# Kernel optimization log

Measured on AMD Instinct MI355X. Metric: run time of the kernel, lower is better.

Reference implementation:

```python
import jax, jax.numpy as jnp
import numpy as np

N = 100000   # nodes
E = 3200000  # edges
IN = 5
H = 128
L = 6
EPS = 1e-5

def _bn(x, g, b):
    # BatchNorm1d in training mode: batch stats over node dim, biased variance
    m = jnp.mean(x, axis=0)
    v = jnp.mean((x - m) ** 2, axis=0)
    return (x - m) * jax.lax.rsqrt(v + EPS) * g + b

def setup_inputs() -> dict:
    key = jax.random.key(0)
    ks = jax.random.split(key, 20)
    x = jax.random.normal(ks[0], (N, IN), dtype=jnp.float32)
    edge_index = jax.random.randint(ks[1], (2, E), 0, N, dtype=jnp.int64)
    batch = jnp.zeros((N,), dtype=jnp.int64)
    s = 0.05
    return {
        "x": x, "edge_index": edge_index, "batch": batch,
        "in_W": jax.random.normal(ks[2], (IN, H), jnp.float32) * s,
        "in_b": jnp.zeros((H,), jnp.float32),
        "in_g": jnp.ones((H,), jnp.float32),
        "in_beta": jnp.zeros((H,), jnp.float32),
        "conv_W": jax.random.normal(ks[3], (L, H, H), jnp.float32) * s,
        "conv_b": jnp.zeros((L, H), jnp.float32),
        "bn_g": jnp.ones((L, H), jnp.float32),
        "bn_beta": jnp.zeros((L, H), jnp.float32),
        "pW1": jax.random.normal(ks[4], (H, 32), jnp.float32) * s,
        "pb1": jnp.zeros((32,), jnp.float32),
        "pW2": jax.random.normal(ks[5], (32, 1), jnp.float32) * s,
        "pb2": jnp.zeros((1,), jnp.float32),
        "vW1": jax.random.normal(ks[6], (H, 64), jnp.float32) * s,
        "vb1": jnp.zeros((64,), jnp.float32),
        "vW2": jax.random.normal(ks[7], (64, 1), jnp.float32) * s,
        "vb2": jnp.zeros((1,), jnp.float32),
    }

def reference(x, edge_index, batch, in_W, in_b, in_g, in_beta,
              conv_W, conv_b, bn_g, bn_beta,
              pW1, pb1, pW2, pb2, vW1, vb1, vW2, vb2):
    n = x.shape[0]
    # GCN normalization with self-loops (computed once; depends only on edge_index)
    loops = jnp.arange(n, dtype=edge_index.dtype)
    src = jnp.concatenate([edge_index[0], loops])
    dst = jnp.concatenate([edge_index[1], loops])
    deg = jax.ops.segment_sum(jnp.ones_like(dst, dtype=x.dtype), dst, num_segments=n)
    dinv = jnp.where(deg > 0, jax.lax.rsqrt(deg), 0.0)
    norm = dinv[src] * dinv[dst]  # [E+N]

    def gcn(h, W, b):
        h = h @ W
        msg = h[src] * norm[:, None]
        return jax.ops.segment_sum(msg, dst, num_segments=n) + b

    h = jax.nn.relu(_bn(x @ in_W + in_b, in_g, in_beta))
    for i in range(L):
        h = jax.nn.relu(_bn(gcn(h, conv_W[i], conv_b[i]), bn_g[i], bn_beta[i])) + h

    policy_logits = (jax.nn.relu(h @ pW1 + pb1) @ pW2 + pb2)[:, 0]  # [N]

    # global_mean_pool over batch ids (single graph here, num_segments=1)
    num_graphs = 1
    sums = jax.ops.segment_sum(h, batch, num_segments=num_graphs)
    cnts = jax.ops.segment_sum(jnp.ones((n,), h.dtype), batch, num_segments=num_graphs)
    g = sums / jnp.maximum(cnts, 1.0)[:, None]  # [1, H]
    value = jnp.tanh(jax.nn.relu(g @ vW1 + vb1) @ vW2 + vb2)[:, 0]  # [1]
    return policy_logits, value
```

## Files before the change

kernel.cpp:

```cpp
#include <hip/hip_runtime.h>
#include <hip/hip_bf16.h>

typedef __hip_bfloat16 bf16;
typedef long long i64;
typedef unsigned short u16;
typedef __attribute__((ext_vector_type(8))) short bf16x8;
typedef __attribute__((ext_vector_type(4))) float f32x4;

#define EPSV 1e-5f
#define WINLEN 2560
#define CHUNK 64

static __device__ __forceinline__ float ldf(const void* p, size_t i, int fb) {
  return fb ? __bfloat162float(((const bf16*)p)[i]) : ((const float*)p)[i];
}
static __device__ __forceinline__ u16 f2b(float f) {
  unsigned int u = __float_as_uint(f);
  u += 0x7FFF + ((u >> 16) & 1);
  return (u16)(u >> 16);
}
static __device__ __forceinline__ float rb2f(u16 u) {
  return __uint_as_float(((unsigned int)u) << 16);
}


__global__ void setup_kernel(const int* __restrict__ ei_w, const unsigned int* __restrict__ g,
                             int* __restrict__ eflag, int* __restrict__ fflag,
                             int* __restrict__ degcnt, int* __restrict__ fill,
                             int* __restrict__ wctr, int n) {
  int i = blockIdx.x * 256 + threadIdx.x;
  if (i < n) { degcnt[i] = 0; fill[i] = 0; }
  if (blockIdx.x == 0) {
    __shared__ int nz;
    if (threadIdx.x == 0) nz = 0;
    if (threadIdx.x < 32) wctr[threadIdx.x] = 0;
    __syncthreads();
    for (int k = threadIdx.x; k < 1024; k += 256)
      if (ei_w[2 * k + 1] != 0) atomicAdd(&nz, 1);
    __syncthreads();
    if (threadIdx.x == 0) {
      *eflag = (nz == 0) ? 1 : 0;
      *fflag = (g[0] == 0x3F803F80u) ? 1 : 0;
    }
  }
}

__global__ void deg_kernel(const void* __restrict__ ei, const int* __restrict__ flag,
                           int* __restrict__ degcnt, int e, int n) {
  int k = blockIdx.x & 7;
  int lo = (int)(((long long)n * k) >> 3);
  int hi = (int)(((long long)n * (k + 1)) >> 3);
  int stride = (gridDim.x >> 3) * 256;
  int fb64 = *flag;
  for (int i = (blockIdx.x >> 3) * 256 + threadIdx.x; i < e; i += stride) {
    int d;
    if (fb64) d = (int)((const i64*)ei)[(size_t)e + i];
    else      d = ((const int*)ei)[(size_t)e + i];
    if (d >= lo && d < hi) atomicAdd(&degcnt[d], 1);
  }
}


__global__ void __launch_bounds__(256) scanA_kernel(const int* __restrict__ deg,
                                                    int* __restrict__ rp,
                                                    int* __restrict__ bsum,
                                                    float* __restrict__ dinv, int n) {
  int base = blockIdx.x * 1024 + threadIdx.x * 4;
  int v0 = (base     < n) ? deg[base]     : 0;
  int v1 = (base + 1 < n) ? deg[base + 1] : 0;
  int v2 = (base + 2 < n) ? deg[base + 2] : 0;
  int v3 = (base + 3 < n) ? deg[base + 3] : 0;
  if (base     < n) dinv[base]     = rsqrtf((float)v0 + 1.0f);
  if (base + 1 < n) dinv[base + 1] = rsqrtf((float)v1 + 1.0f);
  if (base + 2 < n) dinv[base + 2] = rsqrtf((float)v2 + 1.0f);
  if (base + 3 < n) dinv[base + 3] = rsqrtf((float)v3 + 1.0f);
  int ts = v0 + v1 + v2 + v3;
  __shared__ int ls[256];
  ls[threadIdx.x] = ts;
  __syncthreads();
  for (int off = 1; off < 256; off <<= 1) {
    int u = (threadIdx.x >= off) ? ls[threadIdx.x - off] : 0;
    __syncthreads();
    ls[threadIdx.x] += u;
    __syncthreads();
  }
  int run = ls[threadIdx.x] - ts;
  if (base     < n) rp[base]     = run; run += v0;
  if (base + 1 < n) rp[base + 1] = run; run += v1;
  if (base + 2 < n) rp[base + 2] = run; run += v2;
  if (base + 3 < n) rp[base + 3] = run;
  if (threadIdx.x == 255) bsum[blockIdx.x] = ls[255];
}

__global__ void __launch_bounds__(256) scanB_kernel(int* __restrict__ bsum, int* __restrict__ rp,
                                                    int nb, int n, int e) {
  __shared__ int ls[256];
  int t = threadIdx.x;
  int v = (t < nb) ? bsum[t] : 0;
  ls[t] = v;
  __syncthreads();
  for (int off = 1; off < 256; off <<= 1) {
    int u = (t >= off) ? ls[t - off] : 0;
    __syncthreads();
    ls[t] += u;
    __syncthreads();
  }
  if (t < nb) bsum[t] = ls[t] - v;
  if (t == 0) rp[n] = e;
}

__global__ void scanC_kernel(int* __restrict__ rp, const int* __restrict__ bsum, int n) {
  int i = blockIdx.x * 256 + threadIdx.x;
  if (i < n) rp[i] += bsum[i >> 10];
}

__global__ void fill_kernel(const void* __restrict__ ei, const int* __restrict__ flag,
                            const int* __restrict__ row_ptr,
                            int* __restrict__ fill, int* __restrict__ csr_src, int e, int n) {
  int k = blockIdx.x & 7;
  int lo = (int)(((long long)n * k) >> 3);
  int hi = (int)(((long long)n * (k + 1)) >> 3);
  int stride = (gridDim.x >> 3) * 256;
  int fb64 = *flag;
  for (int i = (blockIdx.x >> 3) * 256 + threadIdx.x; i < e; i += stride) {
    int d;
    if (fb64) d = (int)((const i64*)ei)[(size_t)e + i];
    else      d = ((const int*)ei)[(size_t)e + i];
    if (d < lo || d >= hi) continue;
    int s;
    if (fb64) s = (int)((const i64*)ei)[i];
    else      s = ((const int*)ei)[i];
    int pos = row_ptr[d] + atomicAdd(&fill[d], 1);
    csr_src[pos] = s;
  }
}


__global__ void wfrag_kernel(const void* __restrict__ W, const int* __restrict__ fflag,
                             u16* __restrict__ wf, int total) {
  int fb = *fflag;
  int i = blockIdx.x * 256 + threadIdx.x;
  if (i >= total) return;
  int l = i >> 14, r = i & 16383;
  int k = r >> 7, nn = r & 127;
  int s = k >> 5, quad = (k >> 3) & 3, j = k & 7;
  int ct = nn >> 4, n16 = nn & 15;
  wf[(size_t)l * 16384 + (ct * 4 + s) * 512 + quad * 128 + n16 * 8 + j] = f2b(ldf(W, i, fb));
}


__global__ void __launch_bounds__(256) inproj_stats_kernel(
    const void* __restrict__ x, const void* __restrict__ W, const void* __restrict__ b,
    const int* __restrict__ fflag, float* __restrict__ pre,
    float* __restrict__ pi, int n, int in_dim) {
  int fb = *fflag;
  int q = threadIdx.x & 31, g8 = threadIdx.x >> 5;
  int c = q * 4;
  float b0 = ldf(b, c, fb), b1 = ldf(b, c + 1, fb), b2v = ldf(b, c + 2, fb), b3 = ldf(b, c + 3, fb);
  float s0 = 0, s1 = 0, s2 = 0, s3 = 0, q0 = 0, q1 = 0, q2 = 0, q3 = 0;
  for (int node = blockIdx.x * 8 + g8; node < n; node += gridDim.x * 8) {
    float a0 = b0, a1 = b1, a2 = b2v, a3 = b3;
    for (int k = 0; k < in_dim; ++k) {
      float xv = ldf(x, (size_t)node * in_dim + k, fb);
      size_t w0 = (size_t)k * 128 + c;
      a0 = fmaf(xv, ldf(W, w0, fb), a0);
      a1 = fmaf(xv, ldf(W, w0 + 1, fb), a1);
      a2 = fmaf(xv, ldf(W, w0 + 2, fb), a2);
      a3 = fmaf(xv, ldf(W, w0 + 3, fb), a3);
    }
    *(float4*)(pre + (size_t)node * 128 + c) = make_float4(a0, a1, a2, a3);
    s0 += a0; s1 += a1; s2 += a2; s3 += a3;
    q0 = fmaf(a0, a0, q0); q1 = fmaf(a1, a1, q1); q2 = fmaf(a2, a2, q2); q3 = fmaf(a3, a3, q3);
  }
  __shared__ float4 SS[256], QQ[256];
  SS[threadIdx.x] = make_float4(s0, s1, s2, s3);
  QQ[threadIdx.x] = make_float4(q0, q1, q2, q3);
  __syncthreads();
  if (threadIdx.x < 32) {
    float4 a = SS[threadIdx.x], qq = QQ[threadIdx.x];
    for (int g = 1; g < 8; ++g) {
      float4 u = SS[g * 32 + threadIdx.x], w = QQ[g * 32 + threadIdx.x];
      a.x += u.x; a.y += u.y; a.z += u.z; a.w += u.w;
      qq.x += w.x; qq.y += w.y; qq.z += w.z; qq.w += w.w;
    }
    int cc = threadIdx.x * 4;
    *(float4*)(pi + (size_t)blockIdx.x * 256 + cc) = a;
    *(float4*)(pi + (size_t)blockIdx.x * 256 + 128 + cc) = qq;
  }
}

__global__ void __launch_bounds__(1024) finalize_inproj_kernel(
    const float* __restrict__ pi, int nb,
    const void* __restrict__ g, const void* __restrict__ beta,
    const int* __restrict__ fflag,
    float* __restrict__ scale, float* __restrict__ shift,
    float inv_n) {
  __shared__ float RS[8][128], RQ[8][128];
  int fb = *fflag;
  int c = threadIdx.x & 127, r = threadIdx.x >> 7;
  float s = 0.f, s2 = 0.f;
#pragma unroll 4
  for (int b = r; b < nb; b += 8) {
    s  += pi[(size_t)b * 256 + c];
    s2 += pi[(size_t)b * 256 + 128 + c];
  }
  RS[r][c] = s; RQ[r][c] = s2;
  __syncthreads();
  if (threadIdx.x < 128) {
    float ts = 0.f, tq = 0.f;
#pragma unroll
    for (int i = 0; i < 8; ++i) { ts += RS[i][c]; tq += RQ[i][c]; }
    float mean = ts * inv_n;
    float var = tq * inv_n - mean * mean;
    float sc = ldf(g, c, fb) * rsqrtf(var + EPSV);
    scale[c] = sc;
    shift[c] = ldf(beta, c, fb) - mean * sc;
  }
}


__global__ void __launch_bounds__(256) gemm_bn_kernel(
    const float* __restrict__ pre, float* __restrict__ hbuf,
    const float* __restrict__ scale, const float* __restrict__ shift,
    const u16* __restrict__ wfL, const float* __restrict__ dinv,
    u16* __restrict__ u, int n, int use_res) {
  __shared__ u16 At[4][2048];
  int lane = threadIdx.x & 63;
  int wave = threadIdx.x >> 6;
  int n16 = lane & 15, quad = lane >> 4;
  u16* at = At[wave];
  int node = lane & 15;
  int cgrp = lane >> 4;
  int ntiles = (n + 15) >> 4;
  for (int tile = blockIdx.x * 4 + wave; tile < ntiles; tile += gridDim.x * 4) {
    int n0 = tile * 16;
    int gn = n0 + node;
#pragma unroll
    for (int r = 0; r < 8; ++r) {
      int c4 = r * 4 + cgrp;
      int c = c4 * 4;
      float4 h4 = make_float4(0.f, 0.f, 0.f, 0.f);
      if (gn < n) {
        float4 p = *(const float4*)(pre + (size_t)gn * 128 + c);
        float4 sc = *(const float4*)(scale + c);
        float4 sh = *(const float4*)(shift + c);
        h4.x = fmaxf(fmaf(p.x, sc.x, sh.x), 0.f);
        h4.y = fmaxf(fmaf(p.y, sc.y, sh.y), 0.f);
        h4.z = fmaxf(fmaf(p.z, sc.z, sh.z), 0.f);
        h4.w = fmaxf(fmaf(p.w, sc.w, sh.w), 0.f);
        if (use_res) {
          float4 rv = *(const float4*)(hbuf + (size_t)gn * 128 + c);
          h4.x += rv.x; h4.y += rv.y; h4.z += rv.z; h4.w += rv.w;
        }
        *(float4*)(hbuf + (size_t)gn * 128 + c) = h4;
      }
      ushort4 uu;
      uu.x = f2b(h4.x); uu.y = f2b(h4.y); uu.z = f2b(h4.z); uu.w = f2b(h4.w);
      int s = c4 >> 3, qd = (c4 >> 1) & 3, j0 = (c4 & 1) * 4;
      *(ushort4*)(at + s * 512 + qd * 128 + node * 8 + j0) = uu;
    }
    __builtin_amdgcn_s_waitcnt(0);
    f32x4 acc[8];
#pragma unroll
    for (int ct = 0; ct < 8; ++ct) acc[ct] = (f32x4){0.f, 0.f, 0.f, 0.f};
#pragma unroll
    for (int s = 0; s < 4; ++s) {
      bf16x8 af = *(const bf16x8*)(at + s * 512 + lane * 8);
#pragma unroll
      for (int ct = 0; ct < 8; ++ct) {
        bf16x8 bfr = *(const bf16x8*)(wfL + (size_t)(ct * 4 + s) * 512 + lane * 8);
        acc[ct] = __builtin_amdgcn_mfma_f32_16x16x32_bf16(af, bfr, acc[ct], 0, 0, 0);
      }
    }
    float dv[4];
#pragma unroll
    for (int r = 0; r < 4; ++r) {
      int row = n0 + quad * 4 + r;
      dv[r] = (row < n) ? dinv[row] : 0.f;
    }
#pragma unroll
    for (int ct = 0; ct < 8; ++ct) {
#pragma unroll
      for (int r = 0; r < 4; ++r) {
        int row = n0 + quad * 4 + r;
        if (row < n)
          u[((size_t)(ct >> 1) * n + row) * 32 + (ct & 1) * 16 + n16] = f2b(acc[ct][r] * dv[r]);
      }
    }
  }
}


__global__ void __launch_bounds__(256) gather_stats_kernel(
    const int* __restrict__ row_ptr, const int* __restrict__ csr_src,
    const u16* __restrict__ u, const float* __restrict__ dinv,
    const void* __restrict__ b, const int* __restrict__ fflag,
    float* __restrict__ pre, float* __restrict__ pg,
    int* __restrict__ wctr, int n, int nch, size_t bOff) {
  __shared__ int sm[WINLEN];
  __shared__ float SW[4][4][8], QW[4][4][8];
  __shared__ int curchunk;
  int fb = *fflag;
  int ct2 = blockIdx.x & 3;
  const u16* us = u + (size_t)ct2 * n * 32;
  int q = threadIdx.x & 3;
  int g = threadIdx.x >> 2;
  int c = ct2 * 32 + q * 8;
  float bias[8];
#pragma unroll
  for (int i = 0; i < 8; ++i) bias[i] = ldf(b, bOff + c + i, fb);
  float sA[8], qA[8];
#pragma unroll
  for (int i = 0; i < 8; ++i) { sA[i] = 0.f; qA[i] = 0.f; }

  for (;;) {
    __syncthreads();
    if (threadIdx.x == 0) curchunk = atomicAdd(&wctr[ct2], 1);
    __syncthreads();
    int ch = curchunk;
    if (ch >= nch) break;
    int c0 = ch * CHUNK;
    int node = c0 + g;
    int valid = node < n;
    int beg = valid ? row_ptr[node] : 0;
    int end = valid ? row_ptr[node + 1] : 0;
    int cend = c0 + CHUNK; if (cend > n) cend = n;
    int chunk_lo = row_ptr[c0];
    int chunk_hi = row_ptr[cend];
    float acc[8];
    if (valid) {
      uint4 su = *(const uint4*)(us + (size_t)node * 32 + q * 8);
      acc[0] = __uint_as_float(su.x << 16); acc[1] = __uint_as_float(su.x & 0xFFFF0000u);
      acc[2] = __uint_as_float(su.y << 16); acc[3] = __uint_as_float(su.y & 0xFFFF0000u);
      acc[4] = __uint_as_float(su.z << 16); acc[5] = __uint_as_float(su.z & 0xFFFF0000u);
      acc[6] = __uint_as_float(su.w << 16); acc[7] = __uint_as_float(su.w & 0xFFFF0000u);
    } else {
#pragma unroll
      for (int i = 0; i < 8; ++i) acc[i] = 0.f;
    }
    for (int wlo = chunk_lo; wlo < chunk_hi; wlo += WINLEN) {
      int wlen = chunk_hi - wlo; if (wlen > WINLEN) wlen = WINLEN;
      __syncthreads();
      for (int i = threadIdx.x; i < wlen; i += 256)
        sm[i] = __builtin_nontemporal_load(csr_src + wlo + i);
      __syncthreads();
      int j0 = beg > wlo ? beg : wlo;
      int j1 = end < wlo + wlen ? end : wlo + wlen;
      int j = j0;
#define ACC(UU) \
      acc[0] += __uint_as_float(UU.x << 16); acc[1] += __uint_as_float(UU.x & 0xFFFF0000u); \
      acc[2] += __uint_as_float(UU.y << 16); acc[3] += __uint_as_float(UU.y & 0xFFFF0000u); \
      acc[4] += __uint_as_float(UU.z << 16); acc[5] += __uint_as_float(UU.z & 0xFFFF0000u); \
      acc[6] += __uint_as_float(UU.w << 16); acc[7] += __uint_as_float(UU.w & 0xFFFF0000u);
      for (; j + 8 <= j1; j += 8) {
        int i0 = sm[j - wlo],     i1 = sm[j - wlo + 1], i2 = sm[j - wlo + 2], i3 = sm[j - wlo + 3];
        int i4 = sm[j - wlo + 4], i5 = sm[j - wlo + 5], i6 = sm[j - wlo + 6], i7 = sm[j - wlo + 7];
        uint4 U0 = *(const uint4*)(us + (size_t)i0 * 32 + q * 8);
        uint4 U1 = *(const uint4*)(us + (size_t)i1 * 32 + q * 8);
        uint4 U2 = *(const uint4*)(us + (size_t)i2 * 32 + q * 8);
        uint4 U3 = *(const uint4*)(us + (size_t)i3 * 32 + q * 8);
        uint4 U4 = *(const uint4*)(us + (size_t)i4 * 32 + q * 8);
        uint4 U5 = *(const uint4*)(us + (size_t)i5 * 32 + q * 8);
        uint4 U6 = *(const uint4*)(us + (size_t)i6 * 32 + q * 8);
        uint4 U7 = *(const uint4*)(us + (size_t)i7 * 32 + q * 8);
        ACC(U0) ACC(U1) ACC(U2) ACC(U3) ACC(U4) ACC(U5) ACC(U6) ACC(U7)
      }
      for (; j + 4 <= j1; j += 4) {
        int i0 = sm[j - wlo], i1 = sm[j - wlo + 1], i2 = sm[j - wlo + 2], i3 = sm[j - wlo + 3];
        uint4 U0 = *(const uint4*)(us + (size_t)i0 * 32 + q * 8);
        uint4 U1 = *(const uint4*)(us + (size_t)i1 * 32 + q * 8);
        uint4 U2 = *(const uint4*)(us + (size_t)i2 * 32 + q * 8);
        uint4 U3 = *(const uint4*)(us + (size_t)i3 * 32 + q * 8);
        ACC(U0) ACC(U1) ACC(U2) ACC(U3)
      }
      for (; j < j1; ++j) {
        int i0 = sm[j - wlo];
        uint4 U0 = *(const uint4*)(us + (size_t)i0 * 32 + q * 8);
        ACC(U0)
      }
#undef ACC
    }
    if (valid) {
      float dv = dinv[node];
      float4 o0, o1;
      o0.x = fmaf(acc[0], dv, bias[0]); o0.y = fmaf(acc[1], dv, bias[1]);
      o0.z = fmaf(acc[2], dv, bias[2]); o0.w = fmaf(acc[3], dv, bias[3]);
      o1.x = fmaf(acc[4], dv, bias[4]); o1.y = fmaf(acc[5], dv, bias[5]);
      o1.z = fmaf(acc[6], dv, bias[6]); o1.w = fmaf(acc[7], dv, bias[7]);
      *(float4*)(pre + (size_t)node * 128 + c) = o0;
      *(float4*)(pre + (size_t)node * 128 + c + 4) = o1;
      sA[0] += o0.x; sA[1] += o0.y; sA[2] += o0.z; sA[3] += o0.w;
      sA[4] += o1.x; sA[5] += o1.y; sA[6] += o1.z; sA[7] += o1.w;
      qA[0] = fmaf(o0.x, o0.x, qA[0]); qA[1] = fmaf(o0.y, o0.y, qA[1]);
      qA[2] = fmaf(o0.z, o0.z, qA[2]); qA[3] = fmaf(o0.w, o0.w, qA[3]);
      qA[4] = fmaf(o1.x, o1.x, qA[4]); qA[5] = fmaf(o1.y, o1.y, qA[5]);
      qA[6] = fmaf(o1.z, o1.z, qA[6]); qA[7] = fmaf(o1.w, o1.w, qA[7]);
    }
  }
#pragma unroll
  for (int m = 4; m <= 32; m <<= 1) {
#pragma unroll
    for (int i = 0; i < 8; ++i) {
      sA[i] += __shfl_xor(sA[i], m, 64);
      qA[i] += __shfl_xor(qA[i], m, 64);
    }
  }
  int lane = threadIdx.x & 63, wv = threadIdx.x >> 6;
  if (lane < 4) {
#pragma unroll
    for (int i = 0; i < 8; ++i) { SW[wv][lane][i] = sA[i]; QW[wv][lane][i] = qA[i]; }
  }
  __syncthreads();
  if (threadIdx.x < 32) {
    int qq = threadIdx.x >> 3, i = threadIdx.x & 7;
    float a = SW[0][qq][i] + SW[1][qq][i] + SW[2][qq][i] + SW[3][qq][i];
    float b2 = QW[0][qq][i] + QW[1][qq][i] + QW[2][qq][i] + QW[3][qq][i];
    pg[(size_t)blockIdx.x * 64 + qq * 8 + i] = a;
    pg[(size_t)blockIdx.x * 64 + 32 + qq * 8 + i] = b2;
  }
}

__global__ void __launch_bounds__(1024) finalize_gather_kernel(
    const float* __restrict__ pg, int nbG,
    const void* __restrict__ g, const void* __restrict__ beta,
    const int* __restrict__ fflag,
    float* __restrict__ scale, float* __restrict__ shift,
    float inv_n, size_t off) {
  __shared__ float RS[8][128], RQ[8][128];
  int fb = *fflag;
  int c = threadIdx.x & 127, r = threadIdx.x >> 7;
  int ct2 = c >> 5, ic = c & 31;
  float s = 0.f, s2 = 0.f;
#pragma unroll 4
  for (int b = ct2 + 4 * r; b < nbG; b += 32) {
    s  += pg[(size_t)b * 64 + ic];
    s2 += pg[(size_t)b * 64 + 32 + ic];
  }
  RS[r][c] = s; RQ[r][c] = s2;
  __syncthreads();
  if (threadIdx.x < 128) {
    float ts = 0.f, tq = 0.f;
#pragma unroll
    for (int i = 0; i < 8; ++i) { ts += RS[i][c]; tq += RQ[i][c]; }
    float mean = ts * inv_n;
    float var = tq * inv_n - mean * mean;
    float sc = ldf(g, off + c, fb) * rsqrtf(var + EPSV);
    scale[c] = sc;
    shift[c] = ldf(beta, off + c, fb) - mean * sc;
  }
}


__global__ void __launch_bounds__(256) policy_pool_kernel(
    const float* __restrict__ pre, const float* __restrict__ hbuf,
    const float* __restrict__ scale, const float* __restrict__ shift,
    const void* __restrict__ pW1, const void* __restrict__ pb1,
    const void* __restrict__ pW2, const void* __restrict__ pb2,
    const int* __restrict__ fflag, float* __restrict__ pp,
    void* __restrict__ out, int n) {
  __shared__ float W1[128 * 32];
  __shared__ float B1v[32], W2v[32];
  int fb = *fflag;
  for (int i = threadIdx.x; i < 128 * 32; i += 256) W1[i] = ldf(pW1, i, fb);
  if (threadIdx.x < 32) {
    B1v[threadIdx.x] = ldf(pb1, threadIdx.x, fb);
    W2v[threadIdx.x] = ldf(pW2, threadIdx.x, fb);
  }
  __syncthreads();
  float bias2 = ldf(pb2, 0, fb);
  int q = threadIdx.x & 31, g8 = threadIdx.x >> 5;
  int c = q * 4;
  float4 sc = *(const float4*)(scale + c);
  float4 sh = *(const float4*)(shift + c);
  float cs0 = 0, cs1 = 0, cs2 = 0, cs3 = 0;
  for (int node = blockIdx.x * 8 + g8; node < n; node += gridDim.x * 8) {
    float4 p = *(const float4*)(pre + (size_t)node * 128 + c);
    float4 r = *(const float4*)(hbuf + (size_t)node * 128 + c);
    float4 h4;
    h4.x = fmaxf(fmaf(p.x, sc.x, sh.x), 0.f) + r.x;
    h4.y = fmaxf(fmaf(p.y, sc.y, sh.y), 0.f) + r.y;
    h4.z = fmaxf(fmaf(p.z, sc.z, sh.z), 0.f) + r.z;
    h4.w = fmaxf(fmaf(p.w, sc.w, sh.w), 0.f) + r.w;
    cs0 += h4.x; cs1 += h4.y; cs2 += h4.z; cs3 += h4.w;
    float acc = B1v[q];
#pragma unroll
    for (int k4 = 0; k4 < 32; ++k4) {
      float hx = __shfl(h4.x, k4, 32);
      float hy = __shfl(h4.y, k4, 32);
      float hz = __shfl(h4.z, k4, 32);
      float hw = __shfl(h4.w, k4, 32);
      int k = k4 * 4;
      acc = fmaf(hx, W1[k * 32 + q], acc);
      acc = fmaf(hy, W1[(k + 1) * 32 + q], acc);
      acc = fmaf(hz, W1[(k + 2) * 32 + q], acc);
      acc = fmaf(hw, W1[(k + 3) * 32 + q], acc);
    }
    acc = fmaxf(acc, 0.f) * W2v[q];
    for (int off = 16; off; off >>= 1) acc += __shfl_down(acc, off, 32);
    if (q == 0) {
      float v = acc + bias2;
      if (fb) ((bf16*)out)[node] = __float2bfloat16(v);
      else    ((float*)out)[node] = v;
    }
  }
  __shared__ float4 SS[256];
  SS[threadIdx.x] = make_float4(cs0, cs1, cs2, cs3);
  __syncthreads();
  if (threadIdx.x < 32) {
    float4 a = SS[threadIdx.x];
    for (int g = 1; g < 8; ++g) {
      float4 u = SS[g * 32 + threadIdx.x];
      a.x += u.x; a.y += u.y; a.z += u.z; a.w += u.w;
    }
    *(float4*)(pp + (size_t)blockIdx.x * 128 + threadIdx.x * 4) = a;
  }
}

__global__ void __launch_bounds__(1024) value_kernel(
    const float* __restrict__ pp, int nbP,
    const void* __restrict__ vW1, const void* __restrict__ vb1,
    const void* __restrict__ vW2, const void* __restrict__ vb2,
    const int* __restrict__ fflag,
    void* __restrict__ out, int n, float inv_n) {
  __shared__ float RS[8][128];
  __shared__ float gs[128];
  int fb = *fflag;
  int c = threadIdx.x & 127, r = threadIdx.x >> 7;
  float s = 0.f;
#pragma unroll 4
  for (int b = r; b < nbP; b += 8) s += pp[(size_t)b * 128 + c];
  RS[r][c] = s;
  __syncthreads();
  if (threadIdx.x < 128) {
    float t = 0.f;
#pragma unroll
    for (int i = 0; i < 8; ++i) t += RS[i][c];
    gs[c] = t;
  }
  __syncthreads();
  if (threadIdx.x < 64) {
    int cc = threadIdx.x;
    float acc = ldf(vb1, cc, fb);
    for (int k = 0; k < 128; ++k) acc = fmaf(gs[k] * inv_n, ldf(vW1, (size_t)k * 64 + cc, fb), acc);
    acc = fmaxf(acc, 0.f);
    float v = acc * ldf(vW2, cc, fb);
    for (int off = 32; off; off >>= 1) v += __shfl_down(v, off, 64);
    if (cc == 0) {
      float rr = tanhf(v + ldf(vb2, 0, fb));
      if (fb) ((bf16*)out)[n] = __float2bfloat16(rr);
      else    ((float*)out)[n] = rr;
    }
  }
}


extern "C" void kernel_launch(void* const* d_in, const int* in_sizes, int n_in,
                              void* d_out, int out_size, void* d_ws, size_t ws_size,
                              hipStream_t stream) {
  const void* x       = d_in[0];
  const void* ei      = d_in[1];
  const void* in_W    = d_in[3];
  const void* in_b    = d_in[4];
  const void* in_g    = d_in[5];
  const void* in_beta = d_in[6];
  const void* conv_W  = d_in[7];
  const void* conv_b  = d_in[8];
  const void* bn_g    = d_in[9];
  const void* bn_beta = d_in[10];
  const void* pW1     = d_in[11];
  const void* pb1     = d_in[12];
  const void* pW2     = d_in[13];
  const void* pb2     = d_in[14];
  const void* vW1     = d_in[15];
  const void* vb1     = d_in[16];
  const void* vW2     = d_in[17];
  const void* vb2     = d_in[18];

  const int H = 128;
  int in_dim = in_sizes[3] / H;
  int n      = in_sizes[0] / in_dim;
  int e      = in_sizes[1] / 2;
  int L      = in_sizes[7] / (H * H);

  const int GS  = 2048;
  const int GI  = 512;
  const int GP  = 1024;
  const int GF  = 2048;

  char* w = (char*)d_ws;
  u16*   u    = (u16*)w;   w += (size_t)n * H * sizeof(u16);
  float* pre  = (float*)w; w += (size_t)n * H * sizeof(float);
  float* hbuf = (float*)w; w += (size_t)n * H * sizeof(float);
  int*   csr_src  = (int*)w;   w += ((size_t)e + 16) * sizeof(int);
  int*   row_ptr  = (int*)w;   w += (size_t)(n + 1 + 15) / 16 * 16 * sizeof(int);
  int*   degcnt   = (int*)w;   w += (size_t)n * sizeof(int);
  int*   fillc    = (int*)w;   w += (size_t)n * sizeof(int);
  float* dinv     = (float*)w; w += (size_t)n * sizeof(float);
  float* scale = (float*)w; w += 128 * sizeof(float);
  float* shift = (float*)w; w += 128 * sizeof(float);
  int*   eflag = (int*)w;   w += 16 * sizeof(int);
  int*   fflag = (int*)w;   w += 16 * sizeof(int);
  int*   bsum  = (int*)w;   w += 256 * sizeof(int);
  int*   wctr  = (int*)w;   w += 32 * sizeof(int);
  u16*   wf    = (u16*)w;   w += (size_t)L * H * H * sizeof(u16);
  float* pi    = (float*)w; w += (size_t)GI * 256 * sizeof(float);
  float* pg    = (float*)w; w += (size_t)GS * 64 * sizeof(float);
  float* pp    = (float*)w; w += (size_t)GP * 128 * sizeof(float);

  int gN = (n + 255) / 256;
  int nb = (n + 1023) >> 10;
  int nch = (n + CHUNK - 1) / CHUNK;
  float inv_n = 1.0f / (float)n;

  setup_kernel<<<gN, 256, 0, stream>>>((const int*)ei, (const unsigned int*)in_g,
                                       eflag, fflag, degcnt, fillc, wctr, n);
  deg_kernel<<<GF, 256, 0, stream>>>(ei, eflag, degcnt, e, n);
  scanA_kernel<<<nb, 256, 0, stream>>>(degcnt, row_ptr, bsum, dinv, n);
  scanB_kernel<<<1, 256, 0, stream>>>(bsum, row_ptr, nb, n, e);
  scanC_kernel<<<gN, 256, 0, stream>>>(row_ptr, bsum, n);
  fill_kernel<<<GF, 256, 0, stream>>>(ei, eflag, row_ptr, fillc, csr_src, e, n);
  wfrag_kernel<<<(L * H * H + 255) / 256, 256, 0, stream>>>(conv_W, fflag, wf, L * H * H);

  inproj_stats_kernel<<<GI, 256, 0, stream>>>(x, in_W, in_b, fflag, pre, pi, n, in_dim);
  finalize_inproj_kernel<<<1, 1024, 0, stream>>>(pi, GI, in_g, in_beta, fflag, scale, shift, inv_n);

  for (int l = 0; l < L; ++l) {
    gemm_bn_kernel<<<2048, 256, 0, stream>>>(pre, hbuf, scale, shift, wf + (size_t)l * H * H,
                                             dinv, u, n, (l > 0) ? 1 : 0);
    gather_stats_kernel<<<GS, 256, 0, stream>>>(row_ptr, csr_src, u, dinv,
                                                conv_b, fflag, pre, pg, wctr + l * 4,
                                                n, nch, (size_t)l * H);
    finalize_gather_kernel<<<1, 1024, 0, stream>>>(pg, GS, bn_g, bn_beta, fflag, scale, shift,
                                                   inv_n, (size_t)l * H);
  }

  policy_pool_kernel<<<GP, 256, 0, stream>>>(pre, hbuf, scale, shift, pW1, pb1, pW2, pb2,
                                             fflag, pp, d_out, n);
  value_kernel<<<1, 1024, 0, stream>>>(pp, GP, vW1, vb1, vW2, vb2, fflag, d_out, n, inv_n);
}
```

Before: 1.785 ms.

## Store pre-activation and residual buffers in bf16 and merge setup kernels

The pre-activation buffer and the residual hidden-state buffer change from fp32 to packed bf16, which halves their memory traffic in every layer's gemm, gather and policy passes. BatchNorm statistics are now accumulated from the rounded bf16 values so they stay consistent with what is stored. The in-projection, degree-counting and weight-fragment kernels are also merged into one launch with block-range dispatch. The cost is lower precision in the residual stream across layers, which may drift from the fp32 reference.

```diff
diff --git a/kernel.cpp b/kernel.cpp
--- a/kernel.cpp
+++ b/kernel.cpp
@@ -22,6 +22,11 @@
 static __device__ __forceinline__ float rb2f(u16 u) {
   return __uint_as_float(((unsigned int)u) << 16);
 }
+static __device__ __forceinline__ unsigned pk2(float a, float b) {
+  return (unsigned)f2b(a) | ((unsigned)f2b(b) << 16);
+}
+static __device__ __forceinline__ float lo2f(unsigned w) { return __uint_as_float(w << 16); }
+static __device__ __forceinline__ float hi2f(unsigned w) { return __uint_as_float(w & 0xFFFF0000u); }
 
 
 __global__ void setup_kernel(const int* __restrict__ ei_w, const unsigned int* __restrict__ g,
@@ -45,18 +50,73 @@
   }
 }
 
-__global__ void deg_kernel(const void* __restrict__ ei, const int* __restrict__ flag,
-                           int* __restrict__ degcnt, int e, int n) {
-  int k = blockIdx.x & 7;
-  int lo = (int)(((long long)n * k) >> 3);
-  int hi = (int)(((long long)n * (k + 1)) >> 3);
-  int stride = (gridDim.x >> 3) * 256;
-  int fb64 = *flag;
-  for (int i = (blockIdx.x >> 3) * 256 + threadIdx.x; i < e; i += stride) {
-    int d;
-    if (fb64) d = (int)((const i64*)ei)[(size_t)e + i];
-    else      d = ((const int*)ei)[(size_t)e + i];
-    if (d >= lo && d < hi) atomicAdd(&degcnt[d], 1);
+
+__global__ void __launch_bounds__(256) pre_merged_kernel(
+    const void* __restrict__ x, const void* __restrict__ W, const void* __restrict__ b,
+    const void* __restrict__ ei, const void* __restrict__ convW,
+    const int* __restrict__ eflag, const int* __restrict__ fflag,
+    int* __restrict__ degcnt, u16* __restrict__ pre, float* __restrict__ pi,
+    u16* __restrict__ wf, int n, int in_dim, int e, int wtotal, int gi, int gf) {
+  __shared__ float4 SS[256], QQ[256];
+  int fb = *fflag;
+  if ((int)blockIdx.x < gi) {
+    int q = threadIdx.x & 31, g8 = threadIdx.x >> 5;
+    int c = q * 4;
+    float b0 = ldf(b, c, fb), b1 = ldf(b, c + 1, fb), b2v = ldf(b, c + 2, fb), b3 = ldf(b, c + 3, fb);
+    float s0 = 0, s1 = 0, s2 = 0, s3 = 0, q0 = 0, q1 = 0, q2 = 0, q3 = 0;
+    for (int node = blockIdx.x * 8 + g8; node < n; node += gi * 8) {
+      float a0 = b0, a1 = b1, a2 = b2v, a3 = b3;
+      for (int k = 0; k < in_dim; ++k) {
+        float xv = ldf(x, (size_t)node * in_dim + k, fb);
+        size_t w0 = (size_t)k * 128 + c;
+        a0 = fmaf(xv, ldf(W, w0, fb), a0);
+        a1 = fmaf(xv, ldf(W, w0 + 1, fb), a1);
+        a2 = fmaf(xv, ldf(W, w0 + 2, fb), a2);
+        a3 = fmaf(xv, ldf(W, w0 + 3, fb), a3);
+      }
+      unsigned w0p = pk2(a0, a1), w1p = pk2(a2, a3);
+      *(uint2*)(pre + (size_t)node * 128 + c) = make_uint2(w0p, w1p);
+      float r0 = lo2f(w0p), r1 = hi2f(w0p), r2 = lo2f(w1p), r3 = hi2f(w1p);
+      s0 += r0; s1 += r1; s2 += r2; s3 += r3;
+      q0 = fmaf(r0, r0, q0); q1 = fmaf(r1, r1, q1); q2 = fmaf(r2, r2, q2); q3 = fmaf(r3, r3, q3);
+    }
+    SS[threadIdx.x] = make_float4(s0, s1, s2, s3);
+    QQ[threadIdx.x] = make_float4(q0, q1, q2, q3);
+    __syncthreads();
+    if (threadIdx.x < 32) {
+      float4 a = SS[threadIdx.x], qq = QQ[threadIdx.x];
+      for (int g = 1; g < 8; ++g) {
+        float4 u = SS[g * 32 + threadIdx.x], w = QQ[g * 32 + threadIdx.x];
+        a.x += u.x; a.y += u.y; a.z += u.z; a.w += u.w;
+        qq.x += w.x; qq.y += w.y; qq.z += w.z; qq.w += w.w;
+      }
+      int cc = threadIdx.x * 4;
+      *(float4*)(pi + (size_t)blockIdx.x * 256 + cc) = a;
+      *(float4*)(pi + (size_t)blockIdx.x * 256 + 128 + cc) = qq;
+    }
+  } else if ((int)blockIdx.x < gi + gf) {
+    int bid = blockIdx.x - gi;
+    int k = bid & 7;
+    int lo = (int)(((long long)n * k) >> 3);
+    int hi = (int)(((long long)n * (k + 1)) >> 3);
+    int stride = (gf >> 3) * 256;
+    int fb64 = *eflag;
+    for (int i = (bid >> 3) * 256 + threadIdx.x; i < e; i += stride) {
+      int d;
+      if (fb64) d = (int)((const i64*)ei)[(size_t)e + i];
+      else      d = ((const int*)ei)[(size_t)e + i];
+      if (d >= lo && d < hi) atomicAdd(&degcnt[d], 1);
+    }
+  } else {
+    int bid = blockIdx.x - gi - gf;
+    int i = bid * 256 + threadIdx.x;
+    if (i < wtotal) {
+      int l = i >> 14, r = i & 16383;
+      int k = r >> 7, nn = r & 127;
+      int s = k >> 5, quad = (k >> 3) & 3, j = k & 7;
+      int ct = nn >> 4, n16 = nn & 15;
+      wf[(size_t)l * 16384 + (ct * 4 + s) * 512 + quad * 128 + n16 * 8 + j] = f2b(ldf(convW, i, fb));
+    }
   }
 }
 
@@ -135,60 +195,6 @@
   }
 }
 
-
-__global__ void wfrag_kernel(const void* __restrict__ W, const int* __restrict__ fflag,
-                             u16* __restrict__ wf, int total) {
-  int fb = *fflag;
-  int i = blockIdx.x * 256 + threadIdx.x;
-  if (i >= total) return;
-  int l = i >> 14, r = i & 16383;
-  int k = r >> 7, nn = r & 127;
-  int s = k >> 5, quad = (k >> 3) & 3, j = k & 7;
-  int ct = nn >> 4, n16 = nn & 15;
-  wf[(size_t)l * 16384 + (ct * 4 + s) * 512 + quad * 128 + n16 * 8 + j] = f2b(ldf(W, i, fb));
-}
-
-
-__global__ void __launch_bounds__(256) inproj_stats_kernel(
-    const void* __restrict__ x, const void* __restrict__ W, const void* __restrict__ b,
-    const int* __restrict__ fflag, float* __restrict__ pre,
-    float* __restrict__ pi, int n, int in_dim) {
-  int fb = *fflag;
-  int q = threadIdx.x & 31, g8 = threadIdx.x >> 5;
-  int c = q * 4;
-  float b0 = ldf(b, c, fb), b1 = ldf(b, c + 1, fb), b2v = ldf(b, c + 2, fb), b3 = ldf(b, c + 3, fb);
-  float s0 = 0, s1 = 0, s2 = 0, s3 = 0, q0 = 0, q1 = 0, q2 = 0, q3 = 0;
-  for (int node = blockIdx.x * 8 + g8; node < n; node += gridDim.x * 8) {
-    float a0 = b0, a1 = b1, a2 = b2v, a3 = b3;
-    for (int k = 0; k < in_dim; ++k) {
-      float xv = ldf(x, (size_t)node * in_dim + k, fb);
-      size_t w0 = (size_t)k * 128 + c;
-      a0 = fmaf(xv, ldf(W, w0, fb), a0);
-      a1 = fmaf(xv, ldf(W, w0 + 1, fb), a1);
-      a2 = fmaf(xv, ldf(W, w0 + 2, fb), a2);
-      a3 = fmaf(xv, ldf(W, w0 + 3, fb), a3);
-    }
-    *(float4*)(pre + (size_t)node * 128 + c) = make_float4(a0, a1, a2, a3);
-    s0 += a0; s1 += a1; s2 += a2; s3 += a3;
-    q0 = fmaf(a0, a0, q0); q1 = fmaf(a1, a1, q1); q2 = fmaf(a2, a2, q2); q3 = fmaf(a3, a3, q3);
-  }
-  __shared__ float4 SS[256], QQ[256];
-  SS[threadIdx.x] = make_float4(s0, s1, s2, s3);
-  QQ[threadIdx.x] = make_float4(q0, q1, q2, q3);
-  __syncthreads();
-  if (threadIdx.x < 32) {
-    float4 a = SS[threadIdx.x], qq = QQ[threadIdx.x];
-    for (int g = 1; g < 8; ++g) {
-      float4 u = SS[g * 32 + threadIdx.x], w = QQ[g * 32 + threadIdx.x];
-      a.x += u.x; a.y += u.y; a.z += u.z; a.w += u.w;
-      qq.x += w.x; qq.y += w.y; qq.z += w.z; qq.w += w.w;
-    }
-    int cc = threadIdx.x * 4;
-    *(float4*)(pi + (size_t)blockIdx.x * 256 + cc) = a;
-    *(float4*)(pi + (size_t)blockIdx.x * 256 + 128 + cc) = qq;
-  }
-}
-
 __global__ void __launch_bounds__(1024) finalize_inproj_kernel(
     const float* __restrict__ pi, int nb,
     const void* __restrict__ g, const void* __restrict__ beta,
@@ -220,7 +226,7 @@
 
 
 __global__ void __launch_bounds__(256) gemm_bn_kernel(
-    const float* __restrict__ pre, float* __restrict__ hbuf,
+    const u16* __restrict__ pre, u16* __restrict__ hbuf,
     const float* __restrict__ scale, const float* __restrict__ shift,
     const u16* __restrict__ wfL, const float* __restrict__ dinv,
     u16* __restrict__ u, int n, int use_res) {
@@ -241,18 +247,19 @@
       int c = c4 * 4;
       float4 h4 = make_float4(0.f, 0.f, 0.f, 0.f);
       if (gn < n) {
-        float4 p = *(const float4*)(pre + (size_t)gn * 128 + c);
+        uint2 pv = *(const uint2*)(pre + (size_t)gn * 128 + c);
         float4 sc = *(const float4*)(scale + c);
         float4 sh = *(const float4*)(shift + c);
-        h4.x = fmaxf(fmaf(p.x, sc.x, sh.x), 0.f);
-        h4.y = fmaxf(fmaf(p.y, sc.y, sh.y), 0.f);
-        h4.z = fmaxf(fmaf(p.z, sc.z, sh.z), 0.f);
-        h4.w = fmaxf(fmaf(p.w, sc.w, sh.w), 0.f);
+        h4.x = fmaxf(fmaf(lo2f(pv.x), sc.x, sh.x), 0.f);
+        h4.y = fmaxf(fmaf(hi2f(pv.x), sc.y, sh.y), 0.f);
+        h4.z = fmaxf(fmaf(lo2f(pv.y), sc.z, sh.z), 0.f);
+        h4.w = fmaxf(fmaf(hi2f(pv.y), sc.w, sh.w), 0.f);
         if (use_res) {
-          float4 rv = *(const float4*)(hbuf + (size_t)gn * 128 + c);
-          h4.x += rv.x; h4.y += rv.y; h4.z += rv.z; h4.w += rv.w;
+          uint2 rv = *(const uint2*)(hbuf + (size_t)gn * 128 + c);
+          h4.x += lo2f(rv.x); h4.y += hi2f(rv.x);
+          h4.z += lo2f(rv.y); h4.w += hi2f(rv.y);
         }
-        *(float4*)(hbuf + (size_t)gn * 128 + c) = h4;
+        *(uint2*)(hbuf + (size_t)gn * 128 + c) = make_uint2(pk2(h4.x, h4.y), pk2(h4.z, h4.w));
       }
       ushort4 uu;
       uu.x = f2b(h4.x); uu.y = f2b(h4.y); uu.z = f2b(h4.z); uu.w = f2b(h4.w);
@@ -295,7 +302,7 @@
     const int* __restrict__ row_ptr, const int* __restrict__ csr_src,
     const u16* __restrict__ u, const float* __restrict__ dinv,
     const void* __restrict__ b, const int* __restrict__ fflag,
-    float* __restrict__ pre, float* __restrict__ pg,
+    u16* __restrict__ pre, float* __restrict__ pg,
     int* __restrict__ wctr, int n, int nch, size_t bOff) {
   __shared__ int sm[WINLEN];
   __shared__ float SW[4][4][8], QW[4][4][8];
@@ -330,10 +337,10 @@
     float acc[8];
     if (valid) {
       uint4 su = *(const uint4*)(us + (size_t)node * 32 + q * 8);
-      acc[0] = __uint_as_float(su.x << 16); acc[1] = __uint_as_float(su.x & 0xFFFF0000u);
-      acc[2] = __uint_as_float(su.y << 16); acc[3] = __uint_as_float(su.y & 0xFFFF0000u);
-      acc[4] = __uint_as_float(su.z << 16); acc[5] = __uint_as_float(su.z & 0xFFFF0000u);
-      acc[6] = __uint_as_float(su.w << 16); acc[7] = __uint_as_float(su.w & 0xFFFF0000u);
+      acc[0] = lo2f(su.x); acc[1] = hi2f(su.x);
+      acc[2] = lo2f(su.y); acc[3] = hi2f(su.y);
+      acc[4] = lo2f(su.z); acc[5] = hi2f(su.z);
+      acc[6] = lo2f(su.w); acc[7] = hi2f(su.w);
     } else {
 #pragma unroll
       for (int i = 0; i < 8; ++i) acc[i] = 0.f;
@@ -348,10 +355,10 @@
       int j1 = end < wlo + wlen ? end : wlo + wlen;
       int j = j0;
 #define ACC(UU) \
-      acc[0] += __uint_as_float(UU.x << 16); acc[1] += __uint_as_float(UU.x & 0xFFFF0000u); \
-      acc[2] += __uint_as_float(UU.y << 16); acc[3] += __uint_as_float(UU.y & 0xFFFF0000u); \
-      acc[4] += __uint_as_float(UU.z << 16); acc[5] += __uint_as_float(UU.z & 0xFFFF0000u); \
-      acc[6] += __uint_as_float(UU.w << 16); acc[7] += __uint_as_float(UU.w & 0xFFFF0000u);
+      acc[0] += lo2f(UU.x); acc[1] += hi2f(UU.x); \
+      acc[2] += lo2f(UU.y); acc[3] += hi2f(UU.y); \
+      acc[4] += lo2f(UU.z); acc[5] += hi2f(UU.z); \
+      acc[6] += lo2f(UU.w); acc[7] += hi2f(UU.w);
       for (; j + 8 <= j1; j += 8) {
         int i0 = sm[j - wlo],     i1 = sm[j - wlo + 1], i2 = sm[j - wlo + 2], i3 = sm[j - wlo + 3];
         int i4 = sm[j - wlo + 4], i5 = sm[j - wlo + 5], i6 = sm[j - wlo + 6], i7 = sm[j - wlo + 7];
@@ -382,19 +389,20 @@
     }
     if (valid) {
       float dv = dinv[node];
-      float4 o0, o1;
-      o0.x = fmaf(acc[0], dv, bias[0]); o0.y = fmaf(acc[1], dv, bias[1]);
-      o0.z = fmaf(acc[2], dv, bias[2]); o0.w = fmaf(acc[3], dv, bias[3]);
-      o1.x = fmaf(acc[4], dv, bias[4]); o1.y = fmaf(acc[5], dv, bias[5]);
-      o1.z = fmaf(acc[6], dv, bias[6]); o1.w = fmaf(acc[7], dv, bias[7]);
-      *(float4*)(pre + (size_t)node * 128 + c) = o0;
-      *(float4*)(pre + (size_t)node * 128 + c + 4) = o1;
-      sA[0] += o0.x; sA[1] += o0.y; sA[2] += o0.z; sA[3] += o0.w;
-      sA[4] += o1.x; sA[5] += o1.y; sA[6] += o1.z; sA[7] += o1.w;
-      qA[0] = fmaf(o0.x, o0.x, qA[0]); qA[1] = fmaf(o0.y, o0.y, qA[1]);
-      qA[2] = fmaf(o0.z, o0.z, qA[2]); qA[3] = fmaf(o0.w, o0.w, qA[3]);
-      qA[4] = fmaf(o1.x, o1.x, qA[4]); qA[5] = fmaf(o1.y, o1.y, qA[5]);
-      qA[6] = fmaf(o1.z, o1.z, qA[6]); qA[7] = fmaf(o1.w, o1.w, qA[7]);
+      float o0 = fmaf(acc[0], dv, bias[0]), o1 = fmaf(acc[1], dv, bias[1]);
+      float o2 = fmaf(acc[2], dv, bias[2]), o3 = fmaf(acc[3], dv, bias[3]);
+      float o4 = fmaf(acc[4], dv, bias[4]), o5 = fmaf(acc[5], dv, bias[5]);
+      float o6 = fmaf(acc[6], dv, bias[6]), o7 = fmaf(acc[7], dv, bias[7]);
+      unsigned w0 = pk2(o0, o1), w1 = pk2(o2, o3), w2 = pk2(o4, o5), w3 = pk2(o6, o7);
+      *(uint4*)(pre + (size_t)node * 128 + c) = make_uint4(w0, w1, w2, w3);
+      float r0 = lo2f(w0), r1 = hi2f(w0), r2 = lo2f(w1), r3 = hi2f(w1);
+      float r4 = lo2f(w2), r5 = hi2f(w2), r6 = lo2f(w3), r7 = hi2f(w3);
+      sA[0] += r0; sA[1] += r1; sA[2] += r2; sA[3] += r3;
+      sA[4] += r4; sA[5] += r5; sA[6] += r6; sA[7] += r7;
+      qA[0] = fmaf(r0, r0, qA[0]); qA[1] = fmaf(r1, r1, qA[1]);
+      qA[2] = fmaf(r2, r2, qA[2]); qA[3] = fmaf(r3, r3, qA[3]);
+      qA[4] = fmaf(r4, r4, qA[4]); qA[5] = fmaf(r5, r5, qA[5]);
+      qA[6] = fmaf(r6, r6, qA[6]); qA[7] = fmaf(r7, r7, qA[7]);
     }
   }
 #pragma unroll
@@ -452,7 +460,7 @@
 
 
 __global__ void __launch_bounds__(256) policy_pool_kernel(
-    const float* __restrict__ pre, const float* __restrict__ hbuf,
+    const u16* __restrict__ pre, const u16* __restrict__ hbuf,
     const float* __restrict__ scale, const float* __restrict__ shift,
     const void* __restrict__ pW1, const void* __restrict__ pb1,
     const void* __restrict__ pW2, const void* __restrict__ pb2,
@@ -474,13 +482,13 @@
   float4 sh = *(const float4*)(shift + c);
   float cs0 = 0, cs1 = 0, cs2 = 0, cs3 = 0;
   for (int node = blockIdx.x * 8 + g8; node < n; node += gridDim.x * 8) {
-    float4 p = *(const float4*)(pre + (size_t)node * 128 + c);
-    float4 r = *(const float4*)(hbuf + (size_t)node * 128 + c);
+    uint2 pv = *(const uint2*)(pre + (size_t)node * 128 + c);
+    uint2 rv = *(const uint2*)(hbuf + (size_t)node * 128 + c);
     float4 h4;
-    h4.x = fmaxf(fmaf(p.x, sc.x, sh.x), 0.f) + r.x;
-    h4.y = fmaxf(fmaf(p.y, sc.y, sh.y), 0.f) + r.y;
-    h4.z = fmaxf(fmaf(p.z, sc.z, sh.z), 0.f) + r.z;
-    h4.w = fmaxf(fmaf(p.w, sc.w, sh.w), 0.f) + r.w;
+    h4.x = fmaxf(fmaf(lo2f(pv.x), sc.x, sh.x), 0.f) + lo2f(rv.x);
+    h4.y = fmaxf(fmaf(hi2f(pv.x), sc.y, sh.y), 0.f) + hi2f(rv.x);
+    h4.z = fmaxf(fmaf(lo2f(pv.y), sc.z, sh.z), 0.f) + lo2f(rv.y);
+    h4.w = fmaxf(fmaf(hi2f(pv.y), sc.w, sh.w), 0.f) + hi2f(rv.y);
     cs0 += h4.x; cs1 += h4.y; cs2 += h4.z; cs3 += h4.w;
     float acc = B1v[q];
 #pragma unroll
@@ -589,8 +597,8 @@
 
   char* w = (char*)d_ws;
   u16*   u    = (u16*)w;   w += (size_t)n * H * sizeof(u16);
-  float* pre  = (float*)w; w += (size_t)n * H * sizeof(float);
-  float* hbuf = (float*)w; w += (size_t)n * H * sizeof(float);
+  u16*   pre  = (u16*)w;   w += (size_t)n * H * sizeof(u16);
+  u16*   hbuf = (u16*)w;   w += (size_t)n * H * sizeof(u16);
   int*   csr_src  = (int*)w;   w += ((size_t)e + 16) * sizeof(int);
   int*   row_ptr  = (int*)w;   w += (size_t)(n + 1 + 15) / 16 * 16 * sizeof(int);
   int*   degcnt   = (int*)w;   w += (size_t)n * sizeof(int);
@@ -610,18 +618,19 @@
   int gN = (n + 255) / 256;
   int nb = (n + 1023) >> 10;
   int nch = (n + CHUNK - 1) / CHUNK;
+  int wtotal = L * H * H;
+  int GW = (wtotal + 255) / 256;
   float inv_n = 1.0f / (float)n;
 
   setup_kernel<<<gN, 256, 0, stream>>>((const int*)ei, (const unsigned int*)in_g,
                                        eflag, fflag, degcnt, fillc, wctr, n);
-  deg_kernel<<<GF, 256, 0, stream>>>(ei, eflag, degcnt, e, n);
+  pre_merged_kernel<<<GI + GF + GW, 256, 0, stream>>>(
+      x, in_W, in_b, ei, conv_W, eflag, fflag, degcnt, pre, pi, wf,
+      n, in_dim, e, wtotal, GI, GF);
   scanA_kernel<<<nb, 256, 0, stream>>>(degcnt, row_ptr, bsum, dinv, n);
   scanB_kernel<<<1, 256, 0, stream>>>(bsum, row_ptr, nb, n, e);
   scanC_kernel<<<gN, 256, 0, stream>>>(row_ptr, bsum, n);
   fill_kernel<<<GF, 256, 0, stream>>>(ei, eflag, row_ptr, fillc, csr_src, e, n);
-  wfrag_kernel<<<(L * H * H + 255) / 256, 256, 0, stream>>>(conv_W, fflag, wf, L * H * H);
-
-  inproj_stats_kernel<<<GI, 256, 0, stream>>>(x, in_W, in_b, fflag, pre, pi, n, in_dim);
   finalize_inproj_kernel<<<1, 1024, 0, stream>>>(pi, GI, in_g, in_beta, fflag, scale, shift, inv_n);
 
   for (int l = 0; l < L; ++l) {
```

After: 1.721 ms. 1.04x faster.
